# Kernel optimization log

Hardware: AMD Instinct MI355X
Metric: run time of the kernel (lower is better)

The kernel has to match this reference:

```python
import jax, jax.numpy as jnp
import numpy as np

DEPTH = 8
LEAVES = 2 ** DEPTH            # 256 leaf values
N_NODES = 2 ** DEPTH - 1       # 255 internal split nodes
TEMP = 1.0
EPS_P = 1e-5
EPS_V = 1e-10
EPS_MASK = 1e-12


def setup_inputs() -> dict:
    key = jax.random.key(0)
    k1, k2, k3 = jax.random.split(key, 3)
    B, D, O = 8192, 512, 64
    x = jax.random.normal(k1, (B, D), dtype=jnp.float32)
    # BaseSplitter assumed: single linear layer + temperature sigmoid
    Ws = jax.random.normal(k2, (D, N_NODES), dtype=jnp.float32) * (1.0 / np.sqrt(D))
    bs = jnp.zeros((N_NODES,), dtype=jnp.float32)
    # xavier_uniform_ init for leaf value table (LEAVES, O)
    limit = float(np.sqrt(6.0 / (LEAVES + O)))
    value = jax.random.uniform(k3, (LEAVES, O), dtype=jnp.float32, minval=-limit, maxval=limit)
    return {"x": x, "Ws": Ws, "bs": bs, "value": value}


def _sdt_forward(x, Ws, bs, value):
    B = x.shape[0]
    leaves = value.shape[0]
    # splitter: per-node routing probabilities, shape (B, 2^depth - 1)
    probs = jax.nn.sigmoid((x @ Ws + bs) / TEMP)

    accum = jnp.zeros((B, leaves), dtype=jnp.float32)
    reg = jnp.float32(0.0)
    for d in range(DEPTH):  # small fixed loop over tree depth
        s, e = 2 ** d - 1, 2 ** (d + 1) - 1
        p = probs[:, s:e]                     # (B, 2^d) nodes at depth d
        logp = jnp.log(jnp.clip(p, EPS_P))
        log1mp = jnp.log(jnp.clip(1.0 - p, EPS_P))
        # regularization: sum over nodes of mean over batch
        reg = reg + (-0.5) * (2.0 ** (-d)) * jnp.log(jnp.clip(p * (1.0 - p), EPS_P)).mean(axis=0).sum()
        # interleave [logp_i, log1mp_i] per node, then broadcast each entry
        # over its span of leaves/2^(d+1) leaf slots
        contrib = jnp.stack([logp, log1mp], axis=-1).reshape(B, 2 ** (d + 1))
        rep = leaves // (2 ** (d + 1))
        accum = accum + jnp.broadcast_to(contrib[:, :, None], (B, 2 ** (d + 1), rep)).reshape(B, leaves)

    sign = jnp.sign(value)                                    # (L, O)
    logval = jnp.log(jnp.clip(jnp.abs(value), EPS_V))          # (L, O)
    ret = logval[None, :, :] + accum[:, :, None]               # (B, L, O)
    log_pos = jax.nn.logsumexp(ret + jnp.log((sign > 0).astype(jnp.float32) + EPS_MASK), axis=1)
    log_neg = jax.nn.logsumexp(ret + jnp.log((sign < 0).astype(jnp.float32) + EPS_MASK), axis=1)
    out = jnp.exp(log_pos) - jnp.exp(log_neg)                  # (B, O)
    return out, reg


def reference(x, Ws, bs, value):
    return _sdt_forward(x, Ws, bs, value)
```

## Files before the change

### kernel.cpp

```cpp
#include <hip/hip_runtime.h>


typedef __attribute__((ext_vector_type(8))) _Float16 half8;
typedef __attribute__((ext_vector_type(4))) _Float16 half4;
typedef __attribute__((ext_vector_type(4))) float floatx4;

constexpr int O = 64;
constexpr int XSTR = 520;
constexpr int PSTR = 280;
constexpr int LSTR = 260;

__global__ __launch_bounds__(256) void sdt_pre(
    const float* __restrict__ Ws, const float* __restrict__ value,
    _Float16* __restrict__ wt, _Float16* __restrict__ vt,
    float* __restrict__ reg_slot)
{
  const int bid = blockIdx.x, t = threadIdx.x;
  if (bid < 64) {
    const int k0 = bid * 8;
    const int n = t;
    const int T = n >> 4, r = n & 15;
    const int c = k0 >> 5, q = (k0 >> 3) & 3;
    _Float16 v8[8];
#pragma unroll
    for (int kk = 0; kk < 8; ++kk) {
      float f = (n < 255) ? Ws[(size_t)(k0 + kk) * 255 + n] : 0.f;
      v8[kk] = (_Float16)f;
    }
    *(half8*)&wt[(size_t)(T * 16 + c) * 512 + (q * 16 + r) * 8] = *(half8*)v8;
  } else {
    const int k0 = (bid - 64) * 64;
#pragma unroll
    for (int j = 0; j < 16; ++j) {
      int e = t + j * 256;
      int k = k0 + (e >> 6), n = e & 63;
      float f = value[(size_t)k * O + n];
      int T = n >> 4, r = n & 15, kc = k >> 5, q = (k >> 3) & 3, jj = k & 7;
      vt[(size_t)(T * 8 + kc) * 512 + (q * 16 + r) * 8 + jj] = (_Float16)f;
    }
    if (bid == 64 && t == 0) *reg_slot = 0.f;
  }
}

__global__ __launch_bounds__(512, 2) void sdt_main(
    const float* __restrict__ x, const _Float16* __restrict__ wt,
    const _Float16* __restrict__ vt, const float* __restrict__ bs,
    float* __restrict__ out, float* __restrict__ reg_out)
{
  __shared__ __align__(16) char smem[33280 + 17920];
  _Float16* xh_s = (_Float16*)smem;
  float*    L_s  = (float*)smem;
  _Float16* P_h  = (_Float16*)(smem + 33280);
  __shared__ float red_s[8];

  const int t = threadIdx.x, lane = t & 63, w = t >> 6;
  const int q = lane >> 4, r16 = lane & 15;
  const int R0 = blockIdx.x * 32;

  {
    const int row = t >> 4, l4 = (t & 15) * 4;
    const float* xrow = x + (size_t)(R0 + row) * 512;
#pragma unroll
    for (int i = 0; i < 8; ++i) {
      const int k = l4 + i * 64;
      float4 v = *(const float4*)(xrow + k);
      half4 h = {(_Float16)v.x, (_Float16)v.y, (_Float16)v.z, (_Float16)v.w};
      *(half4*)&xh_s[row * XSTR + k] = h;
    }
  }
  __syncthreads();

  const _Float16* pb0 = wt + (size_t)(2 * w) * 16 * 512 + lane * 8;
  const _Float16* pb1 = wt + (size_t)(2 * w + 1) * 16 * 512 + lane * 8;
  const int a0off = r16 * XSTR, a1off = (16 + r16) * XSTR;

  floatx4 acc00 = {0,0,0,0}, acc01 = {0,0,0,0}, acc10 = {0,0,0,0}, acc11 = {0,0,0,0};
  half8 B0 = *(const half8*)pb0, B1 = *(const half8*)pb1;

#pragma unroll
  for (int c = 0; c < 16; ++c) {
    half8 n0, n1;
    if (c < 15) {
      n0 = *(const half8*)(pb0 + (c + 1) * 512);
      n1 = *(const half8*)(pb1 + (c + 1) * 512);
    }
    half8 a0 = *(const half8*)&xh_s[a0off + c * 32 + q * 8];
    half8 a1 = *(const half8*)&xh_s[a1off + c * 32 + q * 8];
    acc00 = __builtin_amdgcn_mfma_f32_16x16x32_f16(a0, B0, acc00, 0, 0, 0);
    acc01 = __builtin_amdgcn_mfma_f32_16x16x32_f16(a0, B1, acc01, 0, 0, 0);
    acc10 = __builtin_amdgcn_mfma_f32_16x16x32_f16(a1, B0, acc10, 0, 0, 0);
    acc11 = __builtin_amdgcn_mfma_f32_16x16x32_f16(a1, B1, acc11, 0, 0, 0);
    if (c < 15) { B0 = n0; B1 = n1; }
  }
  __syncthreads();

  {
    const int c0 = w * 32 + r16, c1 = c0 + 16;
#pragma unroll
    for (int r = 0; r < 4; ++r) {
      int row0 = q * 4 + r, row1 = row0 + 16;
      L_s[row0 * LSTR + c0] = acc00[r];
      L_s[row0 * LSTR + c1] = acc01[r];
      L_s[row1 * LSTR + c0] = acc10[r];
      L_s[row1 * LSTR + c1] = acc11[r];
    }
  }
  __syncthreads();

  {
    const int col = t & 255, half = t >> 8;
    float rsum = 0.f;
    if (col < 255) {
      float b = bs[col];
      for (int r = half * 16; r < half * 16 + 16; ++r) {
        float z = L_s[r * LSTR + col] + b;
        float p = 1.f / (1.f + __expf(-z));
        L_s[r * LSTR + col] = p;
        rsum += __logf(fmaxf(p * (1.f - p), 1e-5f));
      }
      int dd = 31 - __clz(col + 1);
      rsum *= -0.5f / (8192.0f * (float)(1 << dd));
    }
#pragma unroll
    for (int off = 32; off; off >>= 1) rsum += __shfl_down(rsum, off, 64);
    if (lane == 0) red_s[w] = rsum;
  }
  __syncthreads();
  if (t == 0) {
    float s = 0.f;
#pragma unroll
    for (int i = 0; i < 8; ++i) s += red_s[i];
    atomicAdd(reg_out, s);
  }

  {
    const int g8 = t & 31, rp = t >> 5;
    const int Lb = g8 * 8;
#pragma unroll
    for (int rr = 0; rr < 2; ++rr) {
      const int row = rp * 2 + rr;
      const float* Lr = &L_s[row * LSTR];
      float pre = 1.f;
#pragma unroll
      for (int dd = 0; dd < 5; ++dd) {
        float p = Lr[(1 << dd) - 1 + (Lb >> (8 - dd))];
        float br = ((Lb >> (7 - dd)) & 1) ? (1.f - p) : p;
        pre *= fmaxf(br, 1e-5f);
      }
      float p5 = Lr[31 + g8];
      float s5a = fmaxf(p5, 1e-5f), s5b = fmaxf(1.f - p5, 1e-5f);
      float p6a = Lr[63 + 2 * g8], p6b = Lr[63 + 2 * g8 + 1];
      float p7v[4];
#pragma unroll
      for (int m = 0; m < 4; ++m) p7v[m] = Lr[127 + 4 * g8 + m];
      _Float16 ph[8];
#pragma unroll
      for (int j = 0; j < 8; ++j) {
        float s5 = (j & 4) ? s5b : s5a;
        float p6 = (j & 4) ? p6b : p6a;
        float s6 = fmaxf((j & 2) ? (1.f - p6) : p6, 1e-5f);
        float p7 = p7v[j >> 1];
        float s7 = fmaxf((j & 1) ? (1.f - p7) : p7, 1e-5f);
        ph[j] = (_Float16)(pre * s5 * s6 * s7);
      }
      *(half8*)&P_h[row * PSTR + Lb] = *(half8*)ph;
    }
  }
  __syncthreads();

  {
    const int tm = w & 1, tn = w >> 1;
    floatx4 C = {0, 0, 0, 0};
    const _Float16* vb = vt + (size_t)(tn * 8) * 512 + lane * 8;
    const _Float16* pa = &P_h[(tm * 16 + r16) * PSTR + q * 8];
#pragma unroll
    for (int kc = 0; kc < 8; ++kc) {
      half8 A8 = *(const half8*)(pa + kc * 32);
      half8 B8 = *(const half8*)(vb + kc * 512);
      C = __builtin_amdgcn_mfma_f32_16x16x32_f16(A8, B8, C, 0, 0, 0);
    }
    const int col = tn * 16 + r16;
#pragma unroll
    for (int r = 0; r < 4; ++r) {
      int row = tm * 16 + q * 4 + r;
      out[(size_t)(R0 + row) * O + col] = C[r];
    }
  }
}

extern "C" void kernel_launch(void* const* d_in, const int* in_sizes, int n_in,
                              void* d_out, int out_size, void* d_ws, size_t ws_size,
                              hipStream_t stream) {
  const float* x     = (const float*)d_in[0];
  const float* Ws    = (const float*)d_in[1];
  const float* bs    = (const float*)d_in[2];
  const float* value = (const float*)d_in[3];
  float* outp = (float*)d_out;
  float* reg_slot = outp + (size_t)8192 * O;
  _Float16* wt = (_Float16*)d_ws;
  _Float16* vt = wt + 256 * 512;

  sdt_pre<<<68, 256, 0, stream>>>(Ws, value, wt, vt, reg_slot);
  sdt_main<<<256, 512, 0, stream>>>(x, wt, vt, bs, outp, reg_slot);
}
```

Before: 83.60 us.

## Halve row tile, fuse sigmoid into GEMM registers, prefetch weights early

Blocks shrink from 32 to 16 rows with 256 threads, and twice as many blocks are launched. Each wave now computes a 16x64 slice of the splitter GEMM with double-buffered A/B register prefetch. Weight loads are issued before the x staging so they overlap it. Sigmoid and the regularizer sum are computed directly on the accumulators instead of going through a shared-memory round trip, and the leaf-value fragments are preloaded into registers before the second GEMM. Smaller tiles give more parallelism and hide latency, but each block reloads the full Ws and value tables, which doubles global/L2 traffic for weights and raises register pressure.

```diff
diff --git a/kernel.cpp b/kernel.cpp
--- a/kernel.cpp
+++ b/kernel.cpp
@@ -42,20 +42,25 @@
   }
 }
 
-__global__ __launch_bounds__(512, 2) void sdt_main(
+__global__ __launch_bounds__(256, 2) void sdt_main(
     const float* __restrict__ x, const _Float16* __restrict__ wt,
     const _Float16* __restrict__ vt, const float* __restrict__ bs,
     float* __restrict__ out, float* __restrict__ reg_out)
 {
-  __shared__ __align__(16) char smem[33280 + 17920];
+  __shared__ __align__(16) char smem[16640 + 8960];
   _Float16* xh_s = (_Float16*)smem;
   float*    L_s  = (float*)smem;
-  _Float16* P_h  = (_Float16*)(smem + 33280);
-  __shared__ float red_s[8];
+  _Float16* P_h  = (_Float16*)(smem + 16640);
+  __shared__ float red_s[4];
 
   const int t = threadIdx.x, lane = t & 63, w = t >> 6;
   const int q = lane >> 4, r16 = lane & 15;
-  const int R0 = blockIdx.x * 32;
+  const int R0 = blockIdx.x * 16;
+
+  const _Float16* pb = wt + (size_t)(w * 4) * 16 * 512 + lane * 8;
+  half8 Ba[4], Bb[4];
+#pragma unroll
+  for (int nt = 0; nt < 4; ++nt) Ba[nt] = *(const half8*)(pb + nt * 16 * 512);
 
   {
     const int row = t >> 4, l4 = (t & 15) * 4;
@@ -68,69 +73,81 @@
       *(half4*)&xh_s[row * XSTR + k] = h;
     }
   }
-  __syncthreads();
-
-  const _Float16* pb0 = wt + (size_t)(2 * w) * 16 * 512 + lane * 8;
-  const _Float16* pb1 = wt + (size_t)(2 * w + 1) * 16 * 512 + lane * 8;
-  const int a0off = r16 * XSTR, a1off = (16 + r16) * XSTR;
-
-  floatx4 acc00 = {0,0,0,0}, acc01 = {0,0,0,0}, acc10 = {0,0,0,0}, acc11 = {0,0,0,0};
-  half8 B0 = *(const half8*)pb0, B1 = *(const half8*)pb1;
-
-#pragma unroll
-  for (int c = 0; c < 16; ++c) {
-    half8 n0, n1;
-    if (c < 15) {
-      n0 = *(const half8*)(pb0 + (c + 1) * 512);
-      n1 = *(const half8*)(pb1 + (c + 1) * 512);
-    }
-    half8 a0 = *(const half8*)&xh_s[a0off + c * 32 + q * 8];
-    half8 a1 = *(const half8*)&xh_s[a1off + c * 32 + q * 8];
-    acc00 = __builtin_amdgcn_mfma_f32_16x16x32_f16(a0, B0, acc00, 0, 0, 0);
-    acc01 = __builtin_amdgcn_mfma_f32_16x16x32_f16(a0, B1, acc01, 0, 0, 0);
-    acc10 = __builtin_amdgcn_mfma_f32_16x16x32_f16(a1, B0, acc10, 0, 0, 0);
-    acc11 = __builtin_amdgcn_mfma_f32_16x16x32_f16(a1, B1, acc11, 0, 0, 0);
-    if (c < 15) { B0 = n0; B1 = n1; }
-  }
-  __syncthreads();
-
-  {
-    const int c0 = w * 32 + r16, c1 = c0 + 16;
+
+#pragma unroll
+  for (int nt = 0; nt < 4; ++nt) Bb[nt] = *(const half8*)(pb + nt * 16 * 512 + 512);
+
+  __syncthreads();
+
+  floatx4 acc[4] = {{0,0,0,0},{0,0,0,0},{0,0,0,0},{0,0,0,0}};
+  const int aoff = r16 * XSTR + q * 8;
+  half8 A0 = *(const half8*)&xh_s[aoff];
+  half8 A1 = *(const half8*)&xh_s[aoff + 32];
+
+#pragma unroll
+  for (int cc = 0; cc < 8; ++cc) {
+    const int c0 = 2 * cc, c1 = 2 * cc + 1;
+#pragma unroll
+    for (int nt = 0; nt < 4; ++nt)
+      acc[nt] = __builtin_amdgcn_mfma_f32_16x16x32_f16(A0, Ba[nt], acc[nt], 0, 0, 0);
+    if (c0 + 2 < 16) {
+      A0 = *(const half8*)&xh_s[aoff + (c0 + 2) * 32];
+#pragma unroll
+      for (int nt = 0; nt < 4; ++nt)
+        Ba[nt] = *(const half8*)(pb + nt * 16 * 512 + (c0 + 2) * 512);
+    }
+#pragma unroll
+    for (int nt = 0; nt < 4; ++nt)
+      acc[nt] = __builtin_amdgcn_mfma_f32_16x16x32_f16(A1, Bb[nt], acc[nt], 0, 0, 0);
+    if (c1 + 2 < 16) {
+      A1 = *(const half8*)&xh_s[aoff + (c1 + 2) * 32];
+#pragma unroll
+      for (int nt = 0; nt < 4; ++nt)
+        Bb[nt] = *(const half8*)(pb + nt * 16 * 512 + (c1 + 2) * 512);
+    }
+  }
+
+  float pv[4][4];
+  float rsum = 0.f;
+#pragma unroll
+  for (int nt = 0; nt < 4; ++nt) {
+    const int col = w * 64 + nt * 16 + r16;
+    const float b = (col < 255) ? bs[col] : 0.f;
+    float csum = 0.f;
 #pragma unroll
     for (int r = 0; r < 4; ++r) {
-      int row0 = q * 4 + r, row1 = row0 + 16;
-      L_s[row0 * LSTR + c0] = acc00[r];
-      L_s[row0 * LSTR + c1] = acc01[r];
-      L_s[row1 * LSTR + c0] = acc10[r];
-      L_s[row1 * LSTR + c1] = acc11[r];
-    }
-  }
-  __syncthreads();
-
-  {
-    const int col = t & 255, half = t >> 8;
-    float rsum = 0.f;
-    if (col < 255) {
-      float b = bs[col];
-      for (int r = half * 16; r < half * 16 + 16; ++r) {
-        float z = L_s[r * LSTR + col] + b;
-        float p = 1.f / (1.f + __expf(-z));
-        L_s[r * LSTR + col] = p;
-        rsum += __logf(fmaxf(p * (1.f - p), 1e-5f));
-      }
-      int dd = 31 - __clz(col + 1);
-      rsum *= -0.5f / (8192.0f * (float)(1 << dd));
-    }
-#pragma unroll
-    for (int off = 32; off; off >>= 1) rsum += __shfl_down(rsum, off, 64);
+      float p = 1.f / (1.f + __expf(-(acc[nt][r] + b)));
+      pv[nt][r] = p;
+      csum += __logf(fmaxf(p * (1.f - p), 1e-5f));
+    }
+    const int dd = 31 - __clz(col + 1);
+    rsum += (col < 255) ? csum * (-0.5f / (8192.0f * (float)(1 << dd))) : 0.f;
+  }
+#pragma unroll
+  for (int off = 32; off; off >>= 1) rsum += __shfl_down(rsum, off, 64);
+
+  __syncthreads();
+
+  {
+#pragma unroll
+    for (int nt = 0; nt < 4; ++nt) {
+      const int col = w * 64 + nt * 16 + r16;
+#pragma unroll
+      for (int r = 0; r < 4; ++r)
+        L_s[(q * 4 + r) * LSTR + col] = pv[nt][r];
+    }
     if (lane == 0) red_s[w] = rsum;
   }
   __syncthreads();
-  if (t == 0) {
-    float s = 0.f;
-#pragma unroll
-    for (int i = 0; i < 8; ++i) s += red_s[i];
-    atomicAdd(reg_out, s);
+
+  if (t == 0)
+    atomicAdd(reg_out, red_s[0] + red_s[1] + red_s[2] + red_s[3]);
+
+  half8 VB[8];
+  {
+    const _Float16* vb = vt + (size_t)(w * 8) * 512 + lane * 8;
+#pragma unroll
+    for (int kc = 0; kc < 8; ++kc) VB[kc] = *(const half8*)(vb + kc * 512);
   }
 
   {
@@ -169,22 +186,17 @@
   __syncthreads();
 
   {
-    const int tm = w & 1, tn = w >> 1;
     floatx4 C = {0, 0, 0, 0};
-    const _Float16* vb = vt + (size_t)(tn * 8) * 512 + lane * 8;
-    const _Float16* pa = &P_h[(tm * 16 + r16) * PSTR + q * 8];
+    const _Float16* pa = &P_h[r16 * PSTR + q * 8];
 #pragma unroll
     for (int kc = 0; kc < 8; ++kc) {
       half8 A8 = *(const half8*)(pa + kc * 32);
-      half8 B8 = *(const half8*)(vb + kc * 512);
-      C = __builtin_amdgcn_mfma_f32_16x16x32_f16(A8, B8, C, 0, 0, 0);
-    }
-    const int col = tn * 16 + r16;
-#pragma unroll
-    for (int r = 0; r < 4; ++r) {
-      int row = tm * 16 + q * 4 + r;
-      out[(size_t)(R0 + row) * O + col] = C[r];
-    }
+      C = __builtin_amdgcn_mfma_f32_16x16x32_f16(A8, VB[kc], C, 0, 0, 0);
+    }
+    const int colo = w * 16 + r16;
+#pragma unroll
+    for (int r = 0; r < 4; ++r)
+      out[(size_t)(R0 + q * 4 + r) * O + colo] = C[r];
   }
 }
 
@@ -201,5 +213,5 @@
   _Float16* vt = wt + 256 * 512;
 
   sdt_pre<<<68, 256, 0, stream>>>(Ws, value, wt, vt, reg_slot);
-  sdt_main<<<256, 512, 0, stream>>>(x, wt, vt, bs, outp, reg_slot);
+  sdt_main<<<512, 256, 0, stream>>>(x, wt, vt, bs, outp, reg_slot);
 }
```

Measured after the change: 88.66 us. 1.06x slower.

## Fuse weight preprocessing into main kernel via cooperative grid sync

Applied to the files above, without the earlier changes.

Merges the weight/value conversion pre-kernel into the main kernel, using a cooperative launch with a grid-wide sync after the first 68 blocks write the transposed fp16 weights, so one kernel launch is removed. The sigmoid and regularizer math now runs directly on the MFMA accumulators in registers before they are stored to shared memory, which drops one shared-memory round trip and one block barrier. The value-table fragments are prefetched into registers before the probability product stage. The cost is a grid barrier that requires all 256 blocks to be co-resident, plus the extra overhead of a cooperative launch.

```diff
diff --git a/kernel.cpp b/kernel.cpp
--- a/kernel.cpp
+++ b/kernel.cpp
@@ -1,50 +1,22 @@
 #include <hip/hip_runtime.h>
+#include <hip/hip_cooperative_groups.h>
 
 
 typedef __attribute__((ext_vector_type(8))) _Float16 half8;
 typedef __attribute__((ext_vector_type(4))) _Float16 half4;
 typedef __attribute__((ext_vector_type(4))) float floatx4;
+
+namespace cg = cooperative_groups;
 
 constexpr int O = 64;
 constexpr int XSTR = 520;
 constexpr int PSTR = 280;
 constexpr int LSTR = 260;
 
-__global__ __launch_bounds__(256) void sdt_pre(
-    const float* __restrict__ Ws, const float* __restrict__ value,
+__global__ __launch_bounds__(512, 2) void sdt_fused(
+    const float* __restrict__ x, const float* __restrict__ Ws,
+    const float* __restrict__ bs, const float* __restrict__ value,
     _Float16* __restrict__ wt, _Float16* __restrict__ vt,
-    float* __restrict__ reg_slot)
-{
-  const int bid = blockIdx.x, t = threadIdx.x;
-  if (bid < 64) {
-    const int k0 = bid * 8;
-    const int n = t;
-    const int T = n >> 4, r = n & 15;
-    const int c = k0 >> 5, q = (k0 >> 3) & 3;
-    _Float16 v8[8];
-#pragma unroll
-    for (int kk = 0; kk < 8; ++kk) {
-      float f = (n < 255) ? Ws[(size_t)(k0 + kk) * 255 + n] : 0.f;
-      v8[kk] = (_Float16)f;
-    }
-    *(half8*)&wt[(size_t)(T * 16 + c) * 512 + (q * 16 + r) * 8] = *(half8*)v8;
-  } else {
-    const int k0 = (bid - 64) * 64;
-#pragma unroll
-    for (int j = 0; j < 16; ++j) {
-      int e = t + j * 256;
-      int k = k0 + (e >> 6), n = e & 63;
-      float f = value[(size_t)k * O + n];
-      int T = n >> 4, r = n & 15, kc = k >> 5, q = (k >> 3) & 3, jj = k & 7;
-      vt[(size_t)(T * 8 + kc) * 512 + (q * 16 + r) * 8 + jj] = (_Float16)f;
-    }
-    if (bid == 64 && t == 0) *reg_slot = 0.f;
-  }
-}
-
-__global__ __launch_bounds__(512, 2) void sdt_main(
-    const float* __restrict__ x, const _Float16* __restrict__ wt,
-    const _Float16* __restrict__ vt, const float* __restrict__ bs,
     float* __restrict__ out, float* __restrict__ reg_out)
 {
   __shared__ __align__(16) char smem[33280 + 17920];
@@ -55,7 +27,8 @@
 
   const int t = threadIdx.x, lane = t & 63, w = t >> 6;
   const int q = lane >> 4, r16 = lane & 15;
-  const int R0 = blockIdx.x * 32;
+  const int bid = blockIdx.x;
+  const int R0 = bid * 32;
 
   {
     const int row = t >> 4, l4 = (t & 15) * 4;
@@ -68,7 +41,36 @@
       *(half4*)&xh_s[row * XSTR + k] = h;
     }
   }
-  __syncthreads();
+  if (bid < 64) {
+    if (t < 256) {
+      const int k0 = bid * 8;
+      const int n = t;
+      const int T = n >> 4, rr = n & 15;
+      const int c = k0 >> 5, qq = (k0 >> 3) & 3;
+      _Float16 v8[8];
+#pragma unroll
+      for (int kk = 0; kk < 8; ++kk) {
+        float f = (n < 255) ? Ws[(size_t)(k0 + kk) * 255 + n] : 0.f;
+        v8[kk] = (_Float16)f;
+      }
+      *(half8*)&wt[(size_t)(T * 16 + c) * 512 + (qq * 16 + rr) * 8] = *(half8*)v8;
+    }
+  } else if (bid < 68) {
+    if (t < 256) {
+      const int k0 = (bid - 64) * 64;
+#pragma unroll
+      for (int j = 0; j < 16; ++j) {
+        int e = t + j * 256;
+        int k = k0 + (e >> 6), n = e & 63;
+        float f = value[(size_t)k * O + n];
+        int T = n >> 4, rr = n & 15, kc = k >> 5, qq = (k >> 3) & 3, jj = k & 7;
+        vt[(size_t)(T * 8 + kc) * 512 + (qq * 16 + rr) * 8 + jj] = (_Float16)f;
+      }
+      if (bid == 64 && t == 0) *reg_out = 0.f;
+    }
+  }
+  __threadfence();
+  cg::this_grid().sync();
 
   const _Float16* pb0 = wt + (size_t)(2 * w) * 16 * 512 + lane * 8;
   const _Float16* pb1 = wt + (size_t)(2 * w + 1) * 16 * 512 + lane * 8;
@@ -92,45 +94,66 @@
     acc11 = __builtin_amdgcn_mfma_f32_16x16x32_f16(a1, B1, acc11, 0, 0, 0);
     if (c < 15) { B0 = n0; B1 = n1; }
   }
+
+  const int c0 = w * 32 + r16, c1 = c0 + 16;
+  float pv00[4], pv01[4], pv10[4], pv11[4];
+  float s0 = 0.f, s1 = 0.f;
+  {
+    const float b0 = bs[c0];
+    const float b1 = (c1 < 255) ? bs[c1] : 0.f;
+#pragma unroll
+    for (int r = 0; r < 4; ++r) {
+      float p;
+      p = 1.f / (1.f + __expf(-(acc00[r] + b0))); pv00[r] = p;
+      s0 += __logf(fmaxf(p * (1.f - p), 1e-5f));
+      p = 1.f / (1.f + __expf(-(acc10[r] + b0))); pv10[r] = p;
+      s0 += __logf(fmaxf(p * (1.f - p), 1e-5f));
+      p = 1.f / (1.f + __expf(-(acc01[r] + b1))); pv01[r] = p;
+      s1 += __logf(fmaxf(p * (1.f - p), 1e-5f));
+      p = 1.f / (1.f + __expf(-(acc11[r] + b1))); pv11[r] = p;
+      s1 += __logf(fmaxf(p * (1.f - p), 1e-5f));
+    }
+  }
+  float rsum;
+  {
+    const int d0 = 31 - __clz(c0 + 1);
+    rsum = s0 * (-0.5f / (8192.0f * (float)(1 << d0)));
+    if (c1 < 255) {
+      const int d1 = 31 - __clz(c1 + 1);
+      rsum += s1 * (-0.5f / (8192.0f * (float)(1 << d1)));
+    }
+  }
+#pragma unroll
+  for (int off = 32; off; off >>= 1) rsum += __shfl_down(rsum, off, 64);
+
   __syncthreads();
 
   {
-    const int c0 = w * 32 + r16, c1 = c0 + 16;
 #pragma unroll
     for (int r = 0; r < 4; ++r) {
-      int row0 = q * 4 + r, row1 = row0 + 16;
-      L_s[row0 * LSTR + c0] = acc00[r];
-      L_s[row0 * LSTR + c1] = acc01[r];
-      L_s[row1 * LSTR + c0] = acc10[r];
-      L_s[row1 * LSTR + c1] = acc11[r];
-    }
+      const int row0 = q * 4 + r, row1 = row0 + 16;
+      L_s[row0 * LSTR + c0] = pv00[r];
+      L_s[row0 * LSTR + c1] = pv01[r];
+      L_s[row1 * LSTR + c0] = pv10[r];
+      L_s[row1 * LSTR + c1] = pv11[r];
+    }
+    if (lane == 0) red_s[w] = rsum;
   }
   __syncthreads();
 
-  {
-    const int col = t & 255, half = t >> 8;
-    float rsum = 0.f;
-    if (col < 255) {
-      float b = bs[col];
-      for (int r = half * 16; r < half * 16 + 16; ++r) {
-        float z = L_s[r * LSTR + col] + b;
-        float p = 1.f / (1.f + __expf(-z));
-        L_s[r * LSTR + col] = p;
-        rsum += __logf(fmaxf(p * (1.f - p), 1e-5f));
-      }
-      int dd = 31 - __clz(col + 1);
-      rsum *= -0.5f / (8192.0f * (float)(1 << dd));
-    }
-#pragma unroll
-    for (int off = 32; off; off >>= 1) rsum += __shfl_down(rsum, off, 64);
-    if (lane == 0) red_s[w] = rsum;
-  }
-  __syncthreads();
   if (t == 0) {
     float s = 0.f;
 #pragma unroll
     for (int i = 0; i < 8; ++i) s += red_s[i];
     atomicAdd(reg_out, s);
+  }
+
+  half8 VB[8];
+  {
+    const int tn = w >> 1;
+    const _Float16* vb = vt + (size_t)(tn * 8) * 512 + lane * 8;
+#pragma unroll
+    for (int kc = 0; kc < 8; ++kc) VB[kc] = *(const half8*)(vb + kc * 512);
   }
 
   {
@@ -171,13 +194,11 @@
   {
     const int tm = w & 1, tn = w >> 1;
     floatx4 C = {0, 0, 0, 0};
-    const _Float16* vb = vt + (size_t)(tn * 8) * 512 + lane * 8;
     const _Float16* pa = &P_h[(tm * 16 + r16) * PSTR + q * 8];
 #pragma unroll
     for (int kc = 0; kc < 8; ++kc) {
       half8 A8 = *(const half8*)(pa + kc * 32);
-      half8 B8 = *(const half8*)(vb + kc * 512);
-      C = __builtin_amdgcn_mfma_f32_16x16x32_f16(A8, B8, C, 0, 0, 0);
+      C = __builtin_amdgcn_mfma_f32_16x16x32_f16(A8, VB[kc], C, 0, 0, 0);
     }
     const int col = tn * 16 + r16;
 #pragma unroll
@@ -200,6 +221,8 @@
   _Float16* wt = (_Float16*)d_ws;
   _Float16* vt = wt + 256 * 512;
 
-  sdt_pre<<<68, 256, 0, stream>>>(Ws, value, wt, vt, reg_slot);
-  sdt_main<<<256, 512, 0, stream>>>(x, wt, vt, bs, outp, reg_slot);
+  void* args[] = { (void*)&x, (void*)&Ws, (void*)&bs, (void*)&value,
+                   (void*)&wt, (void*)&vt, (void*)&outp, (void*)&reg_slot };
+  hipLaunchCooperativeKernel((void*)sdt_fused, dim3(256), dim3(512),
+                             args, 0, stream);
 }
```

Result: slower. 160.9 us (+92.5%).
